# Kernel tuning notes

Hardware: AMD Instinct MI355X
Metric: run time of the kernel (lower is better)

## Reference

```python
import jax, jax.numpy as jnp
import numpy as np

N, D = 262144, 64
C, K, NSPLITS = 16, 4 + 12, 4  # K=16 codewords per codebook (2**NSPLITS)
K = 16
M = 16


def setup_inputs() -> dict:
    key = jax.random.key(0)
    k1, k2, k3, k4, k5 = jax.random.split(key, 5)
    A = jax.random.normal(k1, (N, D), dtype=jnp.float32)
    B = jax.random.normal(k2, (M, D), dtype=jnp.float32)
    prototypes = jax.random.normal(k3, (C, K, D), dtype=jnp.float32)
    split_dims = jax.random.randint(k4, (C, NSPLITS), 0, D, dtype=jnp.int32)
    # level i of the binary tree uses 2**i thresholds; pad to 2**(NSPLITS-1)=8
    split_vals = jax.random.normal(k5, (C, NSPLITS, 2 ** (NSPLITS - 1)), dtype=jnp.float32)
    return {"A": A, "B": B, "prototypes": prototypes,
            "split_dims": split_dims, "split_vals": split_vals}


def _encode(A, split_dims, split_vals):
    # Vectorized maddness_encode / apply_hash_function over all C codebooks.
    n = A.shape[0]
    c = split_dims.shape[0]
    nsplits = split_dims.shape[1]
    c_idx = jnp.arange(c)[None, :]                      # [1, C]
    group_ids = jnp.zeros((n, c), dtype=jnp.int32)      # [N, C]
    for i in range(nsplits):                            # fixed tiny loop (4 levels)
        x = A[:, split_dims[:, i]]                      # [N, C] gather of split dim
        vals_i = split_vals[:, i, :]                    # [C, 8]
        v = vals_i[c_idx, group_ids]                    # [N, C] per-group threshold
        group_ids = group_ids * 2 + (x > v).astype(jnp.int32)
    return group_ids                                    # [N, C] in [0, K)


def reference(A, B, prototypes, split_dims, split_vals):
    # 1) encode A rows: binary-tree hash per codebook -> codeword ids
    A_enc = _encode(A, split_dims, split_vals)          # [N, C] int32
    # 2) LUTs: luts[m, c, k] = <B[m], prototypes[c, k]>  (maddness_lut per row)
    luts = jnp.einsum('md,ckd->ckm', B, prototypes)     # [C, K, M]
    # 3) LUT-based accumulate (quantize_lut=False path): sum over codebooks
    c_idx = jnp.arange(luts.shape[0])[None, :]          # [1, C]
    g = luts[c_idx, A_enc]                              # [N, C, M] gathered LUT entries
    out = g.sum(axis=1).T                               # [M, N]
    return out
```

## Files before the change

### kernel.cpp

```cpp
#include <hip/hip_runtime.h>
#include <hip/hip_fp16.h>


#define NROWS 262144
#define DDIM  64
#define TPB   256
#define ROWS  256
#define TILES 2
#define NBLK  512
#define RSTR  65
#define LSTR  24

typedef __attribute__((ext_vector_type(8))) _Float16 half8;
typedef __attribute__((ext_vector_type(4))) unsigned int u32x4;

__global__ __launch_bounds__(256) void lut_build(
    const float* __restrict__ B,
    const float* __restrict__ P,
    _Float16* __restrict__ lutw)
{
    int o = blockIdx.x * 256 + threadIdx.x;
    int m  = o & 15;
    int ck = o >> 4;
    const float4* Bp = (const float4*)(B + m * DDIM);
    const float4* Pp = (const float4*)(P + ck * DDIM);
    float dot = 0.f;
    #pragma unroll
    for (int q = 0; q < 16; ++q) {
        float4 b = Bp[q], p = Pp[q];
        dot += b.x * p.x + b.y * p.y + b.z * p.z + b.w * p.w;
    }
    lutw[o] = (_Float16)dot;
}

__global__ __launch_bounds__(TPB, 2) void maddness_main(
    const float* __restrict__ A,
    const int*   __restrict__ sd,
    const float* __restrict__ sv,
    const _Float16* __restrict__ lutw,
    float* __restrict__ out)
{
    __shared__ float rows_s[ROWS * RSTR];
    __shared__ __align__(16) _Float16 lut_s[256 * LSTR];
    __shared__ float sv_s[512];

    const int t = threadIdx.x;

    {
        const u32x4* src = (const u32x4*)(lutw + t * 16);
        u32x4 q0 = src[0], q1 = src[1];
        *(u32x4*)(lut_s + t * LSTR)     = q0;
        *(u32x4*)(lut_s + t * LSTR + 8) = q1;
    }
    {
        float2 v = ((const float2*)sv)[t];
        ((float2*)sv_s)[t] = v;
    }

    const float4* A4 = (const float4*)A;
    float4 R[16];
    {
        long base = (long)blockIdx.x * (ROWS * DDIM / 4);
        #pragma unroll
        for (int j = 0; j < 16; ++j) R[j] = A4[base + j * TPB + t];
    }

    for (int s = 0; s < TILES; ++s) {
        const int tile = blockIdx.x + s * NBLK;

        __syncthreads();

        #pragma unroll
        for (int j = 0; j < 16; ++j) {
            int f    = j * TPB + t;
            int row  = f >> 4;
            int colq = (f & 15) * 4;
            float* dst = &rows_s[row * RSTR + colq];
            dst[0] = R[j].x; dst[1] = R[j].y; dst[2] = R[j].z; dst[3] = R[j].w;
        }
        if (s + 1 < TILES) {
            long base = (long)(tile + NBLK) * (ROWS * DDIM / 4);
            #pragma unroll
            for (int j = 0; j < 16; ++j) R[j] = A4[base + j * TPB + t];
        }

        __syncthreads();

        half8 aE0 = {0,0,0,0,0,0,0,0}, aE1 = {0,0,0,0,0,0,0,0};
        half8 aO0 = {0,0,0,0,0,0,0,0}, aO1 = {0,0,0,0,0,0,0,0};

        const float* rrow = &rows_s[t * RSTR];

        #pragma unroll
        for (int c = 0; c < 16; ++c) {
            const int sd0 = sd[c*4+0], sd1 = sd[c*4+1];
            const int sd2 = sd[c*4+2], sd3 = sd[c*4+3];
            float x0 = rrow[sd0];
            float x1 = rrow[sd1];
            float x2 = rrow[sd2];
            float x3 = rrow[sd3];

            int g = (x0 > sv_s[c*32]) ? 1 : 0;
            float v1 = sv_s[c*32 + 8 + g];
            g = (g << 1) | ((x1 > v1) ? 1 : 0);
            float v2 = sv_s[c*32 + 16 + g];
            g = (g << 1) | ((x2 > v2) ? 1 : 0);
            float v3 = sv_s[c*32 + 24 + g];
            g = (g << 1) | ((x3 > v3) ? 1 : 0);

            const _Float16* lp = lut_s + (c * 16 + g) * LSTR;
            half8 l0 = *(const half8*)(lp);
            half8 l1 = *(const half8*)(lp + 8);
            if (c & 1) { aO0 += l0; aO1 += l1; }
            else       { aE0 += l0; aE1 += l1; }
        }

        const int n = tile * ROWS + t;
        #pragma unroll
        for (int m = 0; m < 8; ++m) {
            out[(long)m       * NROWS + n] = (float)aE0[m] + (float)aO0[m];
            out[(long)(m + 8) * NROWS + n] = (float)aE1[m] + (float)aO1[m];
        }
    }
}

extern "C" void kernel_launch(void* const* d_in, const int* in_sizes, int n_in,
                              void* d_out, int out_size, void* d_ws, size_t ws_size,
                              hipStream_t stream) {
    const float* A  = (const float*)d_in[0];
    const float* B  = (const float*)d_in[1];
    const float* P  = (const float*)d_in[2];
    const int*   sd = (const int*)d_in[3];
    const float* sv = (const float*)d_in[4];
    float* out = (float*)d_out;
    _Float16* lutw = (_Float16*)d_ws;

    lut_build<<<dim3(16), dim3(256), 0, stream>>>(B, P, lutw);
    maddness_main<<<dim3(NBLK), dim3(TPB), 0, stream>>>(A, sd, sv, lutw, out);
}
```

Measured before the change: 111.7 us.

## Split into encode kernel with packed codes and separate LUT accumulate kernel

The fused kernel is restructured into two kernels. The first encodes rows into packed 4-bit codes using many small 64-thread blocks and builds the LUT inside its first 16 blocks. The second gathers from the LUT and writes the output. This is meant to raise parallelism and occupancy, since the old kernel had only 512 blocks and heavy shared memory use. The cost is writing and then reading an intermediate codes buffer (2MB) and an extra launch.

```diff
diff --git a/kernel.cpp b/kernel.cpp
--- a/kernel.cpp
+++ b/kernel.cpp
@@ -4,46 +4,94 @@
 
 #define NROWS 262144
 #define DDIM  64
-#define TPB   256
-#define ROWS  256
-#define TILES 2
-#define NBLK  512
 #define RSTR  65
 #define LSTR  24
+#define EBLK  4096
+#define ABLK  1024
 
 typedef __attribute__((ext_vector_type(8))) _Float16 half8;
 typedef __attribute__((ext_vector_type(4))) unsigned int u32x4;
 
-__global__ __launch_bounds__(256) void lut_build(
+__global__ __launch_bounds__(64) void encode_kernel(
+    const float* __restrict__ A,
     const float* __restrict__ B,
     const float* __restrict__ P,
-    _Float16* __restrict__ lutw)
+    const int*   __restrict__ sd,
+    const float* __restrict__ sv,
+    _Float16* __restrict__ lutw,
+    uint2* __restrict__ codes)
 {
-    int o = blockIdx.x * 256 + threadIdx.x;
-    int m  = o & 15;
-    int ck = o >> 4;
-    const float4* Bp = (const float4*)(B + m * DDIM);
-    const float4* Pp = (const float4*)(P + ck * DDIM);
-    float dot = 0.f;
+    __shared__ float rows_s[64 * RSTR];
+    __shared__ float sv_s[512];
+    const int t = threadIdx.x;
+
+    ((float4*)sv_s)[t]      = ((const float4*)sv)[t];
+    ((float4*)sv_s)[t + 64] = ((const float4*)sv)[t + 64];
+
+    const float4* A4 = (const float4*)A;
+    long base = (long)blockIdx.x * (64 * DDIM / 4);
+    float4 R[16];
     #pragma unroll
-    for (int q = 0; q < 16; ++q) {
-        float4 b = Bp[q], p = Pp[q];
-        dot += b.x * p.x + b.y * p.y + b.z * p.z + b.w * p.w;
+    for (int j = 0; j < 16; ++j) R[j] = A4[base + j * 64 + t];
+
+    if (blockIdx.x < 16) {
+        const int m = t & 15;
+        const float4* Bp = (const float4*)(B + m * DDIM);
+        float4 brow[16];
+        #pragma unroll
+        for (int q = 0; q < 16; ++q) brow[q] = Bp[q];
+        #pragma unroll
+        for (int i = 0; i < 4; ++i) {
+            int o  = blockIdx.x * 256 + i * 64 + t;
+            int ck = o >> 4;
+            const float4* Pp = (const float4*)(P + ck * DDIM);
+            float dot = 0.f;
+            #pragma unroll
+            for (int q = 0; q < 16; ++q) {
+                float4 p = Pp[q];
+                dot += p.x * brow[q].x + p.y * brow[q].y
+                     + p.z * brow[q].z + p.w * brow[q].w;
+            }
+            lutw[o] = (_Float16)dot;
+        }
     }
-    lutw[o] = (_Float16)dot;
+
+    #pragma unroll
+    for (int j = 0; j < 16; ++j) {
+        int f    = j * 64 + t;
+        int row  = f >> 4;
+        int colq = (f & 15) * 4;
+        float* dst = &rows_s[row * RSTR + colq];
+        dst[0] = R[j].x; dst[1] = R[j].y; dst[2] = R[j].z; dst[3] = R[j].w;
+    }
+    __syncthreads();
+
+    const float* rrow = &rows_s[t * RSTR];
+    unsigned int lo = 0, hi = 0;
+    #pragma unroll
+    for (int c = 0; c < 16; ++c) {
+        const int sd0 = sd[c*4+0], sd1 = sd[c*4+1];
+        const int sd2 = sd[c*4+2], sd3 = sd[c*4+3];
+        float x0 = rrow[sd0];
+        float x1 = rrow[sd1];
+        float x2 = rrow[sd2];
+        float x3 = rrow[sd3];
+        int g = (x0 > sv_s[c*32]) ? 1 : 0;
+        g = (g << 1) | ((x1 > sv_s[c*32 +  8 + g]) ? 1 : 0);
+        g = (g << 1) | ((x2 > sv_s[c*32 + 16 + g]) ? 1 : 0);
+        g = (g << 1) | ((x3 > sv_s[c*32 + 24 + g]) ? 1 : 0);
+        if (c < 8) lo |= (unsigned)g << (4 * c);
+        else       hi |= (unsigned)g << (4 * (c - 8));
+    }
+    codes[blockIdx.x * 64 + t] = make_uint2(lo, hi);
 }
 
-__global__ __launch_bounds__(TPB, 2) void maddness_main(
-    const float* __restrict__ A,
-    const int*   __restrict__ sd,
-    const float* __restrict__ sv,
+__global__ __launch_bounds__(256) void accum_kernel(
+    const uint2* __restrict__ codes,
     const _Float16* __restrict__ lutw,
     float* __restrict__ out)
 {
-    __shared__ float rows_s[ROWS * RSTR];
     __shared__ __align__(16) _Float16 lut_s[256 * LSTR];
-    __shared__ float sv_s[512];
-
     const int t = threadIdx.x;
 
     {
@@ -52,75 +100,37 @@
         *(u32x4*)(lut_s + t * LSTR)     = q0;
         *(u32x4*)(lut_s + t * LSTR + 8) = q1;
     }
-    {
-        float2 v = ((const float2*)sv)[t];
-        ((float2*)sv_s)[t] = v;
+    __syncthreads();
+
+    const int n = blockIdx.x * 256 + t;
+    const uint2 code = codes[n];
+
+    half8 aE0 = {0,0,0,0,0,0,0,0}, aE1 = {0,0,0,0,0,0,0,0};
+    half8 aO0 = {0,0,0,0,0,0,0,0}, aO1 = {0,0,0,0,0,0,0,0};
+
+    #pragma unroll
+    for (int c = 0; c < 8; ++c) {
+        int g = (code.x >> (4 * c)) & 15;
+        const _Float16* lp = lut_s + (c * 16 + g) * LSTR;
+        half8 l0 = *(const half8*)(lp);
+        half8 l1 = *(const half8*)(lp + 8);
+        if (c & 1) { aO0 += l0; aO1 += l1; }
+        else       { aE0 += l0; aE1 += l1; }
+    }
+    #pragma unroll
+    for (int c = 8; c < 16; ++c) {
+        int g = (code.y >> (4 * (c - 8))) & 15;
+        const _Float16* lp = lut_s + (c * 16 + g) * LSTR;
+        half8 l0 = *(const half8*)(lp);
+        half8 l1 = *(const half8*)(lp + 8);
+        if (c & 1) { aO0 += l0; aO1 += l1; }
+        else       { aE0 += l0; aE1 += l1; }
     }
 
-    const float4* A4 = (const float4*)A;
-    float4 R[16];
-    {
-        long base = (long)blockIdx.x * (ROWS * DDIM / 4);
-        #pragma unroll
-        for (int j = 0; j < 16; ++j) R[j] = A4[base + j * TPB + t];
-    }
-
-    for (int s = 0; s < TILES; ++s) {
-        const int tile = blockIdx.x + s * NBLK;
-
-        __syncthreads();
-
-        #pragma unroll
-        for (int j = 0; j < 16; ++j) {
-            int f    = j * TPB + t;
-            int row  = f >> 4;
-            int colq = (f & 15) * 4;
-            float* dst = &rows_s[row * RSTR + colq];
-            dst[0] = R[j].x; dst[1] = R[j].y; dst[2] = R[j].z; dst[3] = R[j].w;
-        }
-        if (s + 1 < TILES) {
-            long base = (long)(tile + NBLK) * (ROWS * DDIM / 4);
-            #pragma unroll
-            for (int j = 0; j < 16; ++j) R[j] = A4[base + j * TPB + t];
-        }
-
-        __syncthreads();
-
-        half8 aE0 = {0,0,0,0,0,0,0,0}, aE1 = {0,0,0,0,0,0,0,0};
-        half8 aO0 = {0,0,0,0,0,0,0,0}, aO1 = {0,0,0,0,0,0,0,0};
-
-        const float* rrow = &rows_s[t * RSTR];
-
-        #pragma unroll
-        for (int c = 0; c < 16; ++c) {
-            const int sd0 = sd[c*4+0], sd1 = sd[c*4+1];
-            const int sd2 = sd[c*4+2], sd3 = sd[c*4+3];
-            float x0 = rrow[sd0];
-            float x1 = rrow[sd1];
-            float x2 = rrow[sd2];
-            float x3 = rrow[sd3];
-
-            int g = (x0 > sv_s[c*32]) ? 1 : 0;
-            float v1 = sv_s[c*32 + 8 + g];
-            g = (g << 1) | ((x1 > v1) ? 1 : 0);
-            float v2 = sv_s[c*32 + 16 + g];
-            g = (g << 1) | ((x2 > v2) ? 1 : 0);
-            float v3 = sv_s[c*32 + 24 + g];
-            g = (g << 1) | ((x3 > v3) ? 1 : 0);
-
-            const _Float16* lp = lut_s + (c * 16 + g) * LSTR;
-            half8 l0 = *(const half8*)(lp);
-            half8 l1 = *(const half8*)(lp + 8);
-            if (c & 1) { aO0 += l0; aO1 += l1; }
-            else       { aE0 += l0; aE1 += l1; }
-        }
-
-        const int n = tile * ROWS + t;
-        #pragma unroll
-        for (int m = 0; m < 8; ++m) {
-            out[(long)m       * NROWS + n] = (float)aE0[m] + (float)aO0[m];
-            out[(long)(m + 8) * NROWS + n] = (float)aE1[m] + (float)aO1[m];
-        }
+    #pragma unroll
+    for (int m = 0; m < 8; ++m) {
+        out[(long)m       * NROWS + n] = (float)aE0[m] + (float)aO0[m];
+        out[(long)(m + 8) * NROWS + n] = (float)aE1[m] + (float)aO1[m];
     }
 }
 
@@ -133,8 +143,10 @@
     const int*   sd = (const int*)d_in[3];
     const float* sv = (const float*)d_in[4];
     float* out = (float*)d_out;
+
     _Float16* lutw = (_Float16*)d_ws;
+    uint2*    codes = (uint2*)((char*)d_ws + 8192);
 
-    lut_build<<<dim3(16), dim3(256), 0, stream>>>(B, P, lutw);
-    maddness_main<<<dim3(NBLK), dim3(TPB), 0, stream>>>(A, sd, sv, lutw, out);
+    encode_kernel<<<dim3(EBLK), dim3(64), 0, stream>>>(A, B, P, sd, sv, lutw, codes);
+    accum_kernel<<<dim3(ABLK), dim3(256), 0, stream>>>(codes, lutw, out);
 }
```

Measured after the change: 109.1 us. 2.3% less time.

## Gather split-dimension values directly from global memory instead of staging rows in LDS

Applied to the files above, without the earlier changes.

Removes the staging of full 64-float A rows through shared memory, along with its register prefetch and double-tile loop. Each thread now reads only the split-dimension scalars of its own row straight from global memory. The launch grows to 1024 blocks of one row-tile each, with the min-blocks launch bound dropped, cutting LDS usage and synchronisation. The trade-off is strided, uncoalesced per-lane loads that rely on L1/L2 to absorb repeated touches of the same row cache lines.

```diff
diff --git a/kernel.cpp b/kernel.cpp
--- a/kernel.cpp
+++ b/kernel.cpp
@@ -4,12 +4,9 @@
 
 #define NROWS 262144
 #define DDIM  64
+#define LSTR  24
 #define TPB   256
-#define ROWS  256
-#define TILES 2
-#define NBLK  512
-#define RSTR  65
-#define LSTR  24
+#define NBLK  1024
 
 typedef __attribute__((ext_vector_type(8))) _Float16 half8;
 typedef __attribute__((ext_vector_type(4))) unsigned int u32x4;
@@ -33,17 +30,15 @@
     lutw[o] = (_Float16)dot;
 }
 
-__global__ __launch_bounds__(TPB, 2) void maddness_main(
+__global__ __launch_bounds__(TPB) void maddness_fused(
     const float* __restrict__ A,
     const int*   __restrict__ sd,
     const float* __restrict__ sv,
     const _Float16* __restrict__ lutw,
     float* __restrict__ out)
 {
-    __shared__ float rows_s[ROWS * RSTR];
     __shared__ __align__(16) _Float16 lut_s[256 * LSTR];
     __shared__ float sv_s[512];
-
     const int t = threadIdx.x;
 
     {
@@ -51,76 +46,41 @@
         u32x4 q0 = src[0], q1 = src[1];
         *(u32x4*)(lut_s + t * LSTR)     = q0;
         *(u32x4*)(lut_s + t * LSTR + 8) = q1;
+        ((float2*)sv_s)[t] = ((const float2*)sv)[t];
     }
-    {
-        float2 v = ((const float2*)sv)[t];
-        ((float2*)sv_s)[t] = v;
+    __syncthreads();
+
+    const int n = blockIdx.x * TPB + t;
+    const float* __restrict__ Arow = A + (size_t)n * DDIM;
+    const int4* __restrict__ sd4 = (const int4*)sd;
+
+    half8 aE0 = {0,0,0,0,0,0,0,0}, aE1 = {0,0,0,0,0,0,0,0};
+    half8 aO0 = {0,0,0,0,0,0,0,0}, aO1 = {0,0,0,0,0,0,0,0};
+
+    #pragma unroll
+    for (int c = 0; c < 16; ++c) {
+        const int4 s4 = sd4[c];
+        float x0 = Arow[s4.x];
+        float x1 = Arow[s4.y];
+        float x2 = Arow[s4.z];
+        float x3 = Arow[s4.w];
+
+        int g = (x0 > sv_s[c*32]) ? 1 : 0;
+        g = (g << 1) | ((x1 > sv_s[c*32 +  8 + g]) ? 1 : 0);
+        g = (g << 1) | ((x2 > sv_s[c*32 + 16 + g]) ? 1 : 0);
+        g = (g << 1) | ((x3 > sv_s[c*32 + 24 + g]) ? 1 : 0);
+
+        const _Float16* lp = lut_s + (c * 16 + g) * LSTR;
+        half8 l0 = *(const half8*)(lp);
+        half8 l1 = *(const half8*)(lp + 8);
+        if (c & 1) { aO0 += l0; aO1 += l1; }
+        else       { aE0 += l0; aE1 += l1; }
     }
 
-    const float4* A4 = (const float4*)A;
-    float4 R[16];
-    {
-        long base = (long)blockIdx.x * (ROWS * DDIM / 4);
-        #pragma unroll
-        for (int j = 0; j < 16; ++j) R[j] = A4[base + j * TPB + t];
-    }
-
-    for (int s = 0; s < TILES; ++s) {
-        const int tile = blockIdx.x + s * NBLK;
-
-        __syncthreads();
-
-        #pragma unroll
-        for (int j = 0; j < 16; ++j) {
-            int f    = j * TPB + t;
-            int row  = f >> 4;
-            int colq = (f & 15) * 4;
-            float* dst = &rows_s[row * RSTR + colq];
-            dst[0] = R[j].x; dst[1] = R[j].y; dst[2] = R[j].z; dst[3] = R[j].w;
-        }
-        if (s + 1 < TILES) {
-            long base = (long)(tile + NBLK) * (ROWS * DDIM / 4);
-            #pragma unroll
-            for (int j = 0; j < 16; ++j) R[j] = A4[base + j * TPB + t];
-        }
-
-        __syncthreads();
-
-        half8 aE0 = {0,0,0,0,0,0,0,0}, aE1 = {0,0,0,0,0,0,0,0};
-        half8 aO0 = {0,0,0,0,0,0,0,0}, aO1 = {0,0,0,0,0,0,0,0};
-
-        const float* rrow = &rows_s[t * RSTR];
-
-        #pragma unroll
-        for (int c = 0; c < 16; ++c) {
-            const int sd0 = sd[c*4+0], sd1 = sd[c*4+1];
-            const int sd2 = sd[c*4+2], sd3 = sd[c*4+3];
-            float x0 = rrow[sd0];
-            float x1 = rrow[sd1];
-            float x2 = rrow[sd2];
-            float x3 = rrow[sd3];
-
-            int g = (x0 > sv_s[c*32]) ? 1 : 0;
-            float v1 = sv_s[c*32 + 8 + g];
-            g = (g << 1) | ((x1 > v1) ? 1 : 0);
-            float v2 = sv_s[c*32 + 16 + g];
-            g = (g << 1) | ((x2 > v2) ? 1 : 0);
-            float v3 = sv_s[c*32 + 24 + g];
-            g = (g << 1) | ((x3 > v3) ? 1 : 0);
-
-            const _Float16* lp = lut_s + (c * 16 + g) * LSTR;
-            half8 l0 = *(const half8*)(lp);
-            half8 l1 = *(const half8*)(lp + 8);
-            if (c & 1) { aO0 += l0; aO1 += l1; }
-            else       { aE0 += l0; aE1 += l1; }
-        }
-
-        const int n = tile * ROWS + t;
-        #pragma unroll
-        for (int m = 0; m < 8; ++m) {
-            out[(long)m       * NROWS + n] = (float)aE0[m] + (float)aO0[m];
-            out[(long)(m + 8) * NROWS + n] = (float)aE1[m] + (float)aO1[m];
-        }
+    #pragma unroll
+    for (int m = 0; m < 8; ++m) {
+        out[(long)m       * NROWS + n] = (float)aE0[m] + (float)aO0[m];
+        out[(long)(m + 8) * NROWS + n] = (float)aE1[m] + (float)aO1[m];
     }
 }
 
@@ -133,8 +93,9 @@
     const int*   sd = (const int*)d_in[3];
     const float* sv = (const float*)d_in[4];
     float* out = (float*)d_out;
+
     _Float16* lutw = (_Float16*)d_ws;
 
     lut_build<<<dim3(16), dim3(256), 0, stream>>>(B, P, lutw);
-    maddness_main<<<dim3(NBLK), dim3(TPB), 0, stream>>>(A, sd, sv, lutw, out);
+    maddness_fused<<<dim3(NBLK), dim3(TPB), 0, stream>>>(A, sd, sv, lutw, out);
 }
```

Result: slower. 144.6 us (+29.5%).
